# Optimization experiments

Hardware: AMD Instinct MI355X
Metric: run time of the kernel (lower is better)

## Reference

```python
import jax, jax.numpy as jnp
import numpy as np

B, H, S, DK = 2, 16, 2048, 64
NEG = jnp.float32(-10000.0)


def setup_inputs() -> dict:
    key = jax.random.key(0)
    kq, kk, kv, km = jax.random.split(key, 4)
    query = jax.random.normal(kq, (B, H, S, DK), dtype=jnp.float32)
    k_ = jax.random.normal(kk, (B, H, S, DK), dtype=jnp.float32)
    value = jax.random.normal(kv, (B, H, S, DK), dtype=jnp.float32)
    mask = (jax.random.uniform(km, (B, 1, S, S)) > 0.5).astype(jnp.float32)
    return {"query": query, "key": k_, "value": value, "mask": mask, "d_k": DK}


def reference(query, key, value, mask, d_k):
    # scores: [B,H,S,S]
    scale = jnp.float32(1.0 / np.sqrt(d_k))
    scores = jnp.einsum('bhqd,bhkd->bhqk', query, key) * scale * mask
    # non-standard masking: keep only strictly positive masked scores
    scores = jnp.where(scores > 0, scores, NEG)
    attn = jax.nn.softmax(scores, axis=-1)
    return jnp.einsum('bhqk,bhkd->bhqd', attn, value)
```

## Files before the change

### kernel.cpp

```cpp
#include <hip/hip_runtime.h>
#include <math.h>

#define S_LEN 2048
#define D_KV  64
#define BQ    128
#define BK    64
#define NT    (S_LEN / BK)

typedef __attribute__((ext_vector_type(8)))  short bh8;
typedef __attribute__((ext_vector_type(4)))  float fx4;
typedef __attribute__((ext_vector_type(16))) float fx16;
typedef __attribute__((ext_vector_type(4)))  unsigned int u32x4;
typedef __attribute__((ext_vector_type(2)))  unsigned int u32x2;

__device__ __forceinline__ unsigned cvt2(float a, float b) {
    unsigned r;
    asm("v_cvt_pk_bf16_f32 %0, %1, %2" : "=v"(r) : "v"(a), "v"(b));
    return r;
}
__device__ __forceinline__ void swap32(unsigned &d, unsigned &s) {
    asm("v_permlane32_swap_b32 %0, %1" : "+v"(d), "+v"(s));
}
__device__ __forceinline__ int swz(int row, int byteoff) {
    return (row << 7) + (byteoff ^ ((row & 7) << 4));
}

__global__ __launch_bounds__(256, 3)
void attn_fwd(const float* __restrict__ Qg, const float* __restrict__ Kg,
              const float* __restrict__ Vg, const float* __restrict__ Mg,
              float* __restrict__ Og)
{
    __shared__ __align__(16) char smem[16384];
    short* kb = (short*)smem;
    short* vb = (short*)(smem + 8192);

    const int tid  = threadIdx.x;
    const int lane = tid & 63;
    const int wave = tid >> 6;
    const int lq   = lane & 31;
    const int hf   = lane >> 5;

    const int flat = blockIdx.x + (int)gridDim.x * blockIdx.y;
    const int nsw  = (flat & 7) * 64 + (flat >> 3);
    const int qt = nsw & 15;
    const int bh = nsw >> 4;
    const int b  = bh >> 4;

    const int qbase = qt * BQ + wave * 32;

    const float* Kp = Kg + (size_t)bh * S_LEN * D_KV;
    const float* Vp = Vg + (size_t)bh * S_LEN * D_KV;
    const float* Qp = Qg + ((size_t)bh * S_LEN + qbase) * D_KV;
    const float* mrow = Mg + (size_t)b * S_LEN * S_LEN
                      + (size_t)(qbase + lq) * S_LEN + hf * 4;

    bh8 qf[4];
#pragma unroll
    for (int ks = 0; ks < 4; ++ks) {
        const float* src = Qp + lq * D_KV + ks * 16 + hf * 8;
        fx4 a0 = *(const fx4*)src;
        fx4 a1 = *(const fx4*)(src + 4);
        u32x4 q4 = { cvt2(a0[0] * 0.125f, a0[1] * 0.125f),
                     cvt2(a0[2] * 0.125f, a0[3] * 0.125f),
                     cvt2(a1[0] * 0.125f, a1[1] * 0.125f),
                     cvt2(a1[2] * 0.125f, a1[3] * 0.125f) };
        qf[ks] = __builtin_bit_cast(bh8, q4);
    }

    const int krow = tid >> 2;
    const int kcol = (tid & 3) << 2;
    const int vd0  = (tid >> 4) << 2;
    const int vk0  = (tid & 15) << 2;

    fx16 o0 = {}, o1 = {};
    float lsum = 0.f;
    fx4 kreg[4], vreg[4];

#pragma unroll
    for (int i = 0; i < 4; ++i)
        kreg[i] = *(const fx4*)(Kp + (size_t)krow * D_KV + kcol + 16 * i);
#pragma unroll
    for (int i = 0; i < 4; ++i)
        vreg[i] = *(const fx4*)(Vp + (size_t)(vk0 + i) * D_KV + vd0);

#pragma unroll 1
    for (int t = 0; t < NT; ++t) {
        const int kt = t * BK;

        fx4 mv0[4];
#pragma unroll
        for (int m = 0; m < 4; ++m)
            mv0[m] = *(const fx4*)(mrow + kt + m * 8);

#pragma unroll
        for (int i = 0; i < 4; ++i) {
            u32x2 w = { cvt2(kreg[i][0], kreg[i][1]),
                        cvt2(kreg[i][2], kreg[i][3]) };
            *(u32x2*)((char*)kb + swz(krow, (kcol << 1) + 32 * i)) = w;
        }
#pragma unroll
        for (int i = 0; i < 4; ++i) {
            u32x2 w = { cvt2(vreg[0][i], vreg[1][i]),
                        cvt2(vreg[2][i], vreg[3][i]) };
            *(u32x2*)((char*)vb + swz(vd0 + i, vk0 << 1)) = w;
        }
        __syncthreads();

        if (t + 1 < NT) {
            const int kn = kt + BK;
#pragma unroll
            for (int i = 0; i < 4; ++i)
                kreg[i] = *(const fx4*)(Kp + (size_t)(kn + krow) * D_KV + kcol + 16 * i);
#pragma unroll
            for (int i = 0; i < 4; ++i)
                vreg[i] = *(const fx4*)(Vp + (size_t)(kn + vk0 + i) * D_KV + vd0);
        }

        fx16 st0 = {}, st1 = {};
        __builtin_amdgcn_s_setprio(1);
#pragma unroll
        for (int ks = 0; ks < 4; ++ks) {
            bh8 k0 = *(const bh8*)((char*)kb + swz(lq,      ks * 32 + hf * 16));
            bh8 k1 = *(const bh8*)((char*)kb + swz(32 + lq, ks * 32 + hf * 16));
            st0 = __builtin_amdgcn_mfma_f32_32x32x16_bf16(k0, qf[ks], st0, 0, 0, 0);
            st1 = __builtin_amdgcn_mfma_f32_32x32x16_bf16(k1, qf[ks], st1, 0, 0, 0);
        }
        __builtin_amdgcn_s_setprio(0);

        fx4 mv1[4];
#pragma unroll
        for (int m = 0; m < 4; ++m)
            mv1[m] = *(const fx4*)(mrow + kt + 32 + m * 8);

        unsigned pkw[16];

#pragma unroll
        for (int m = 0; m < 4; ++m) {
            float tm0 = st0[4*m+0] * mv0[m][0];
            float tm1 = st0[4*m+1] * mv0[m][1];
            float tm2 = st0[4*m+2] * mv0[m][2];
            float tm3 = st0[4*m+3] * mv0[m][3];
            float p0 = tm0 > 0.f ? __expf(tm0) : 0.f;
            float p1 = tm1 > 0.f ? __expf(tm1) : 0.f;
            float p2 = tm2 > 0.f ? __expf(tm2) : 0.f;
            float p3 = tm3 > 0.f ? __expf(tm3) : 0.f;
            lsum += (p0 + p1) + (p2 + p3);
            pkw[m*2+0] = cvt2(p0, p1);
            pkw[m*2+1] = cvt2(p2, p3);
        }

        __builtin_amdgcn_s_setprio(1);
#pragma unroll
        for (int vp = 0; vp < 2; ++vp) {
            unsigned w0 = pkw[vp*4+0], w1 = pkw[vp*4+1];
            unsigned w2 = pkw[vp*4+2], w3 = pkw[vp*4+3];
            swap32(w0, w2); swap32(w1, w3);
            u32x4 pq = { w0, w1, w2, w3 };
            bh8 pb = __builtin_bit_cast(bh8, pq);
            bh8 v0 = *(const bh8*)((char*)vb + swz(lq,      vp * 32 + hf * 16));
            bh8 v1 = *(const bh8*)((char*)vb + swz(32 + lq, vp * 32 + hf * 16));
            o0 = __builtin_amdgcn_mfma_f32_32x32x16_bf16(v0, pb, o0, 0, 0, 0);
            o1 = __builtin_amdgcn_mfma_f32_32x32x16_bf16(v1, pb, o1, 0, 0, 0);
        }
        __builtin_amdgcn_s_setprio(0);

#pragma unroll
        for (int m = 0; m < 4; ++m) {
            float tm0 = st1[4*m+0] * mv1[m][0];
            float tm1 = st1[4*m+1] * mv1[m][1];
            float tm2 = st1[4*m+2] * mv1[m][2];
            float tm3 = st1[4*m+3] * mv1[m][3];
            float p0 = tm0 > 0.f ? __expf(tm0) : 0.f;
            float p1 = tm1 > 0.f ? __expf(tm1) : 0.f;
            float p2 = tm2 > 0.f ? __expf(tm2) : 0.f;
            float p3 = tm3 > 0.f ? __expf(tm3) : 0.f;
            lsum += (p0 + p1) + (p2 + p3);
            pkw[8 + m*2+0] = cvt2(p0, p1);
            pkw[8 + m*2+1] = cvt2(p2, p3);
        }

        __builtin_amdgcn_s_setprio(1);
#pragma unroll
        for (int vp = 2; vp < 4; ++vp) {
            unsigned w0 = pkw[vp*4+0], w1 = pkw[vp*4+1];
            unsigned w2 = pkw[vp*4+2], w3 = pkw[vp*4+3];
            swap32(w0, w2); swap32(w1, w3);
            u32x4 pq = { w0, w1, w2, w3 };
            bh8 pb = __builtin_bit_cast(bh8, pq);
            bh8 v0 = *(const bh8*)((char*)vb + swz(lq,      vp * 32 + hf * 16));
            bh8 v1 = *(const bh8*)((char*)vb + swz(32 + lq, vp * 32 + hf * 16));
            o0 = __builtin_amdgcn_mfma_f32_32x32x16_bf16(v0, pb, o0, 0, 0, 0);
            o1 = __builtin_amdgcn_mfma_f32_32x32x16_bf16(v1, pb, o1, 0, 0, 0);
        }
        __builtin_amdgcn_s_setprio(0);

        __syncthreads();
    }

    lsum += __shfl_xor(lsum, 32);
    const float inv = 1.0f / lsum;

    float* orow = Og + ((size_t)bh * S_LEN + qbase + lq) * D_KV;
#pragma unroll
    for (int m = 0; m < 4; ++m) {
        fx4 r0 = { o0[4*m+0]*inv, o0[4*m+1]*inv, o0[4*m+2]*inv, o0[4*m+3]*inv };
        *(fx4*)(orow + m * 8 + hf * 4) = r0;
        fx4 r1 = { o1[4*m+0]*inv, o1[4*m+1]*inv, o1[4*m+2]*inv, o1[4*m+3]*inv };
        *(fx4*)(orow + 32 + m * 8 + hf * 4) = r1;
    }
}

extern "C" void kernel_launch(void* const* d_in, const int* in_sizes, int n_in,
                              void* d_out, int out_size, void* d_ws, size_t ws_size,
                              hipStream_t stream) {
    const float* Q = (const float*)d_in[0];
    const float* K = (const float*)d_in[1];
    const float* V = (const float*)d_in[2];
    const float* M = (const float*)d_in[3];
    float*       O = (float*)d_out;
    dim3 grid(S_LEN / BQ, 32);
    attn_fwd<<<grid, 256, 0, stream>>>(Q, K, V, M, O);
}
```

Measured before the change: 234.8 us.

## Split KV range across two wave groups with double-buffered LDS and merge

After: 424.6 us. +80.8%, slower.

```diff
diff --git a/kernel.cpp b/kernel.cpp
--- a/kernel.cpp
+++ b/kernel.cpp
@@ -5,7 +5,8 @@
 #define D_KV  64
 #define BQ    128
 #define BK    64
-#define NT    (S_LEN / BK)
+#define KHALF 1024
+#define NT    (KHALF / BK)
 
 typedef __attribute__((ext_vector_type(8)))  short bh8;
 typedef __attribute__((ext_vector_type(4)))  float fx4;
@@ -21,22 +22,27 @@
 __device__ __forceinline__ void swap32(unsigned &d, unsigned &s) {
     asm("v_permlane32_swap_b32 %0, %1" : "+v"(d), "+v"(s));
 }
+__device__ __forceinline__ float exp2_fast(float x) {
+    float r;
+    asm("v_exp_f32 %0, %1" : "=v"(r) : "v"(x));
+    return r;
+}
 __device__ __forceinline__ int swz(int row, int byteoff) {
     return (row << 7) + (byteoff ^ ((row & 7) << 4));
 }
 
-__global__ __launch_bounds__(256, 3)
+__global__ __launch_bounds__(512, 4)
 void attn_fwd(const float* __restrict__ Qg, const float* __restrict__ Kg,
               const float* __restrict__ Vg, const float* __restrict__ Mg,
               float* __restrict__ Og)
 {
-    __shared__ __align__(16) char smem[16384];
-    short* kb = (short*)smem;
-    short* vb = (short*)(smem + 8192);
+    __shared__ __align__(16) char smem[65536];
 
     const int tid  = threadIdx.x;
     const int lane = tid & 63;
     const int wave = tid >> 6;
+    const int qw   = wave & 3;
+    const int kg   = wave >> 2;
     const int lq   = lane & 31;
     const int hf   = lane >> 5;
 
@@ -46,82 +52,91 @@
     const int bh = nsw >> 4;
     const int b  = bh >> 4;
 
-    const int qbase = qt * BQ + wave * 32;
-
-    const float* Kp = Kg + (size_t)bh * S_LEN * D_KV;
-    const float* Vp = Vg + (size_t)bh * S_LEN * D_KV;
+    const int qbase = qt * BQ + qw * 32;
+
+    const float* Kp = Kg + ((size_t)bh * S_LEN + kg * KHALF) * D_KV;
+    const float* Vp = Vg + ((size_t)bh * S_LEN + kg * KHALF) * D_KV;
     const float* Qp = Qg + ((size_t)bh * S_LEN + qbase) * D_KV;
     const float* mrow = Mg + (size_t)b * S_LEN * S_LEN
-                      + (size_t)(qbase + lq) * S_LEN + hf * 4;
-
+                      + (size_t)(qbase + lq) * S_LEN + kg * KHALF + hf * 4;
+
+    const float QS = 0.125f * 1.44269504f;
     bh8 qf[4];
 #pragma unroll
     for (int ks = 0; ks < 4; ++ks) {
         const float* src = Qp + lq * D_KV + ks * 16 + hf * 8;
         fx4 a0 = *(const fx4*)src;
         fx4 a1 = *(const fx4*)(src + 4);
-        u32x4 q4 = { cvt2(a0[0] * 0.125f, a0[1] * 0.125f),
-                     cvt2(a0[2] * 0.125f, a0[3] * 0.125f),
-                     cvt2(a1[0] * 0.125f, a1[1] * 0.125f),
-                     cvt2(a1[2] * 0.125f, a1[3] * 0.125f) };
+        u32x4 q4 = { cvt2(a0[0] * QS, a0[1] * QS),
+                     cvt2(a0[2] * QS, a0[3] * QS),
+                     cvt2(a1[0] * QS, a1[1] * QS),
+                     cvt2(a1[2] * QS, a1[3] * QS) };
         qf[ks] = __builtin_bit_cast(bh8, q4);
     }
 
-    const int krow = tid >> 2;
-    const int kcol = (tid & 3) << 2;
-    const int vd0  = (tid >> 4) << 2;
-    const int vk0  = (tid & 15) << 2;
+    const int stid  = tid & 255;
+    const int krow  = stid >> 2;
+    const int kcolf = (stid & 3) << 2;
+    const int vd0   = (stid >> 4) << 2;
+    const int vk0   = (stid & 15) << 2;
+
+    char* lbase = smem + kg * 32768;
+
+    fx4 kreg[4], vreg[4];
+    auto issue = [&](int t) {
+        const int k0 = t * BK;
+#pragma unroll
+        for (int i = 0; i < 4; ++i)
+            kreg[i] = *(const fx4*)(Kp + (size_t)(k0 + krow) * D_KV + kcolf + 16 * i);
+#pragma unroll
+        for (int i = 0; i < 4; ++i)
+            vreg[i] = *(const fx4*)(Vp + (size_t)(k0 + vk0 + i) * D_KV + vd0);
+    };
+    auto store_kv = [&](int buf) {
+        char* kbW = lbase + buf * 16384;
+        char* vbW = kbW + 8192;
+#pragma unroll
+        for (int i = 0; i < 4; ++i) {
+            u32x2 w = { cvt2(kreg[i][0], kreg[i][1]),
+                        cvt2(kreg[i][2], kreg[i][3]) };
+            *(u32x2*)(kbW + swz(krow, (kcolf << 1) + 32 * i)) = w;
+        }
+#pragma unroll
+        for (int i = 0; i < 4; ++i) {
+            u32x2 w = { cvt2(vreg[0][i], vreg[1][i]),
+                        cvt2(vreg[2][i], vreg[3][i]) };
+            *(u32x2*)(vbW + swz(vd0 + i, vk0 << 1)) = w;
+        }
+    };
 
     fx16 o0 = {}, o1 = {};
     float lsum = 0.f;
-    fx4 kreg[4], vreg[4];
-
-#pragma unroll
-    for (int i = 0; i < 4; ++i)
-        kreg[i] = *(const fx4*)(Kp + (size_t)krow * D_KV + kcol + 16 * i);
-#pragma unroll
-    for (int i = 0; i < 4; ++i)
-        vreg[i] = *(const fx4*)(Vp + (size_t)(vk0 + i) * D_KV + vd0);
+
+    issue(0);
+    store_kv(0);
+    issue(1);
+    asm volatile("s_waitcnt lgkmcnt(0)" ::: "memory");
+    __builtin_amdgcn_s_barrier();
 
 #pragma unroll 1
     for (int t = 0; t < NT; ++t) {
-        const int kt = t * BK;
+        char* kbR = lbase + (t & 1) * 16384;
+        char* vbR = kbR + 8192;
+        const int mc = t * BK;
 
         fx4 mv0[4];
 #pragma unroll
         for (int m = 0; m < 4; ++m)
-            mv0[m] = *(const fx4*)(mrow + kt + m * 8);
-
-#pragma unroll
-        for (int i = 0; i < 4; ++i) {
-            u32x2 w = { cvt2(kreg[i][0], kreg[i][1]),
-                        cvt2(kreg[i][2], kreg[i][3]) };
-            *(u32x2*)((char*)kb + swz(krow, (kcol << 1) + 32 * i)) = w;
-        }
-#pragma unroll
-        for (int i = 0; i < 4; ++i) {
-            u32x2 w = { cvt2(vreg[0][i], vreg[1][i]),
-                        cvt2(vreg[2][i], vreg[3][i]) };
-            *(u32x2*)((char*)vb + swz(vd0 + i, vk0 << 1)) = w;
-        }
-        __syncthreads();
-
-        if (t + 1 < NT) {
-            const int kn = kt + BK;
-#pragma unroll
-            for (int i = 0; i < 4; ++i)
-                kreg[i] = *(const fx4*)(Kp + (size_t)(kn + krow) * D_KV + kcol + 16 * i);
-#pragma unroll
-            for (int i = 0; i < 4; ++i)
-                vreg[i] = *(const fx4*)(Vp + (size_t)(kn + vk0 + i) * D_KV + vd0);
-        }
+            mv0[m] = *(const fx4*)(mrow + mc + m * 8);
+
+        if (t + 1 < NT) store_kv((t + 1) & 1);
 
         fx16 st0 = {}, st1 = {};
         __builtin_amdgcn_s_setprio(1);
 #pragma unroll
         for (int ks = 0; ks < 4; ++ks) {
-            bh8 k0 = *(const bh8*)((char*)kb + swz(lq,      ks * 32 + hf * 16));
-            bh8 k1 = *(const bh8*)((char*)kb + swz(32 + lq, ks * 32 + hf * 16));
+            bh8 k0 = *(const bh8*)(kbR + swz(lq,      ks * 32 + hf * 16));
+            bh8 k1 = *(const bh8*)(kbR + swz(32 + lq, ks * 32 + hf * 16));
             st0 = __builtin_amdgcn_mfma_f32_32x32x16_bf16(k0, qf[ks], st0, 0, 0, 0);
             st1 = __builtin_amdgcn_mfma_f32_32x32x16_bf16(k1, qf[ks], st1, 0, 0, 0);
         }
@@ -130,7 +145,8 @@
         fx4 mv1[4];
 #pragma unroll
         for (int m = 0; m < 4; ++m)
-            mv1[m] = *(const fx4*)(mrow + kt + 32 + m * 8);
+            mv1[m] = *(const fx4*)(mrow + mc + 32 + m * 8);
+        if (t + 2 < NT) issue(t + 2);
 
         unsigned pkw[16];
 
@@ -140,10 +156,10 @@
             float tm1 = st0[4*m+1] * mv0[m][1];
             float tm2 = st0[4*m+2] * mv0[m][2];
             float tm3 = st0[4*m+3] * mv0[m][3];
-            float p0 = tm0 > 0.f ? __expf(tm0) : 0.f;
-            float p1 = tm1 > 0.f ? __expf(tm1) : 0.f;
-            float p2 = tm2 > 0.f ? __expf(tm2) : 0.f;
-            float p3 = tm3 > 0.f ? __expf(tm3) : 0.f;
+            float p0 = tm0 > 0.f ? exp2_fast(tm0) : 0.f;
+            float p1 = tm1 > 0.f ? exp2_fast(tm1) : 0.f;
+            float p2 = tm2 > 0.f ? exp2_fast(tm2) : 0.f;
+            float p3 = tm3 > 0.f ? exp2_fast(tm3) : 0.f;
             lsum += (p0 + p1) + (p2 + p3);
             pkw[m*2+0] = cvt2(p0, p1);
             pkw[m*2+1] = cvt2(p2, p3);
@@ -157,8 +173,8 @@
             swap32(w0, w2); swap32(w1, w3);
             u32x4 pq = { w0, w1, w2, w3 };
             bh8 pb = __builtin_bit_cast(bh8, pq);
-            bh8 v0 = *(const bh8*)((char*)vb + swz(lq,      vp * 32 + hf * 16));
-            bh8 v1 = *(const bh8*)((char*)vb + swz(32 + lq, vp * 32 + hf * 16));
+            bh8 v0 = *(const bh8*)(vbR + swz(lq,      vp * 32 + hf * 16));
+            bh8 v1 = *(const bh8*)(vbR + swz(32 + lq, vp * 32 + hf * 16));
             o0 = __builtin_amdgcn_mfma_f32_32x32x16_bf16(v0, pb, o0, 0, 0, 0);
             o1 = __builtin_amdgcn_mfma_f32_32x32x16_bf16(v1, pb, o1, 0, 0, 0);
         }
@@ -170,10 +186,10 @@
             float tm1 = st1[4*m+1] * mv1[m][1];
             float tm2 = st1[4*m+2] * mv1[m][2];
             float tm3 = st1[4*m+3] * mv1[m][3];
-            float p0 = tm0 > 0.f ? __expf(tm0) : 0.f;
-            float p1 = tm1 > 0.f ? __expf(tm1) : 0.f;
-            float p2 = tm2 > 0.f ? __expf(tm2) : 0.f;
-            float p3 = tm3 > 0.f ? __expf(tm3) : 0.f;
+            float p0 = tm0 > 0.f ? exp2_fast(tm0) : 0.f;
+            float p1 = tm1 > 0.f ? exp2_fast(tm1) : 0.f;
+            float p2 = tm2 > 0.f ? exp2_fast(tm2) : 0.f;
+            float p3 = tm3 > 0.f ? exp2_fast(tm3) : 0.f;
             lsum += (p0 + p1) + (p2 + p3);
             pkw[8 + m*2+0] = cvt2(p0, p1);
             pkw[8 + m*2+1] = cvt2(p2, p3);
@@ -187,26 +203,55 @@
             swap32(w0, w2); swap32(w1, w3);
             u32x4 pq = { w0, w1, w2, w3 };
             bh8 pb = __builtin_bit_cast(bh8, pq);
-            bh8 v0 = *(const bh8*)((char*)vb + swz(lq,      vp * 32 + hf * 16));
-            bh8 v1 = *(const bh8*)((char*)vb + swz(32 + lq, vp * 32 + hf * 16));
+            bh8 v0 = *(const bh8*)(vbR + swz(lq,      vp * 32 + hf * 16));
+            bh8 v1 = *(const bh8*)(vbR + swz(32 + lq, vp * 32 + hf * 16));
             o0 = __builtin_amdgcn_mfma_f32_32x32x16_bf16(v0, pb, o0, 0, 0, 0);
             o1 = __builtin_amdgcn_mfma_f32_32x32x16_bf16(v1, pb, o1, 0, 0, 0);
         }
         __builtin_amdgcn_s_setprio(0);
 
-        __syncthreads();
+        asm volatile("s_waitcnt lgkmcnt(0)" ::: "memory");
+        __builtin_amdgcn_s_barrier();
     }
 
     lsum += __shfl_xor(lsum, 32);
-    const float inv = 1.0f / lsum;
-
-    float* orow = Og + ((size_t)bh * S_LEN + qbase + lq) * D_KV;
-#pragma unroll
-    for (int m = 0; m < 4; ++m) {
-        fx4 r0 = { o0[4*m+0]*inv, o0[4*m+1]*inv, o0[4*m+2]*inv, o0[4*m+3]*inv };
-        *(fx4*)(orow + m * 8 + hf * 4) = r0;
-        fx4 r1 = { o1[4*m+0]*inv, o1[4*m+1]*inv, o1[4*m+2]*inv, o1[4*m+3]*inv };
-        *(fx4*)(orow + 32 + m * 8 + hf * 4) = r1;
+
+    float* scr = (float*)smem;
+    const int slot = qw * 64 + lane;
+    if (kg) {
+        float* d = scr + slot * 36;
+#pragma unroll
+        for (int i = 0; i < 4; ++i) {
+            fx4 c0 = { o0[4*i+0], o0[4*i+1], o0[4*i+2], o0[4*i+3] };
+            *(fx4*)(d + 4 * i) = c0;
+            fx4 c1 = { o1[4*i+0], o1[4*i+1], o1[4*i+2], o1[4*i+3] };
+            *(fx4*)(d + 16 + 4 * i) = c1;
+        }
+        d[32] = lsum;
+    }
+    __syncthreads();
+    if (!kg) {
+        const float* s = scr + slot * 36;
+#pragma unroll
+        for (int i = 0; i < 4; ++i) {
+            fx4 c0 = *(const fx4*)(s + 4 * i);
+            o0[4*i+0] += c0[0]; o0[4*i+1] += c0[1];
+            o0[4*i+2] += c0[2]; o0[4*i+3] += c0[3];
+            fx4 c1 = *(const fx4*)(s + 16 + 4 * i);
+            o1[4*i+0] += c1[0]; o1[4*i+1] += c1[1];
+            o1[4*i+2] += c1[2]; o1[4*i+3] += c1[3];
+        }
+        lsum += s[32];
+        const float inv = 1.0f / lsum;
+
+        float* orow = Og + ((size_t)bh * S_LEN + qbase + lq) * D_KV;
+#pragma unroll
+        for (int m = 0; m < 4; ++m) {
+            fx4 r0 = { o0[4*m+0]*inv, o0[4*m+1]*inv, o0[4*m+2]*inv, o0[4*m+3]*inv };
+            *(fx4*)(orow + m * 8 + hf * 4) = r0;
+            fx4 r1 = { o1[4*m+0]*inv, o1[4*m+1]*inv, o1[4*m+2]*inv, o1[4*m+3]*inv };
+            *(fx4*)(orow + 32 + m * 8 + hf * 4) = r1;
+        }
     }
 }
 
@@ -219,5 +264,5 @@
     const float* M = (const float*)d_in[3];
     float*       O = (float*)d_out;
     dim3 grid(S_LEN / BQ, 32);
-    attn_fwd<<<grid, 256, 0, stream>>>(Q, K, V, M, O);
-}
+    attn_fwd<<<grid, 512, 0, stream>>>(Q, K, V, M, O);
+}
```

## Pack float mask into bitmask via pre-kernel and use exp2 with raw barriers

Applied to the files above, without the earlier changes.

After: 194.7 us. -17.1%, faster.

```diff
diff --git a/kernel.cpp b/kernel.cpp
--- a/kernel.cpp
+++ b/kernel.cpp
@@ -21,13 +21,34 @@
 __device__ __forceinline__ void swap32(unsigned &d, unsigned &s) {
     asm("v_permlane32_swap_b32 %0, %1" : "+v"(d), "+v"(s));
 }
+__device__ __forceinline__ float exp2_fast(float x) {
+    float r;
+    asm("v_exp_f32 %0, %1" : "=v"(r) : "v"(x));
+    return r;
+}
 __device__ __forceinline__ int swz(int row, int byteoff) {
     return (row << 7) + (byteoff ^ ((row & 7) << 4));
 }
 
+__global__ __launch_bounds__(256)
+void pack_mask(const float* __restrict__ M, unsigned long long* __restrict__ BM)
+{
+    const size_t i = (size_t)blockIdx.x * 256 + threadIdx.x;
+    const float v = M[i];
+    const unsigned long long bits = __ballot(v > 0.5f);
+    if ((threadIdx.x & 63) == 0) {
+        const size_t g = i >> 6;
+        const int col64 = (int)(g & 31);
+        const int row   = (int)((g >> 5) & 2047);
+        const int b     = (int)(g >> 16);
+        BM[((size_t)b * 32 + col64) * 2048 + row] = bits;
+    }
+}
+
 __global__ __launch_bounds__(256, 3)
 void attn_fwd(const float* __restrict__ Qg, const float* __restrict__ Kg,
-              const float* __restrict__ Vg, const float* __restrict__ Mg,
+              const float* __restrict__ Vg,
+              const unsigned long long* __restrict__ BMg,
               float* __restrict__ Og)
 {
     __shared__ __align__(16) char smem[16384];
@@ -51,19 +72,19 @@
     const float* Kp = Kg + (size_t)bh * S_LEN * D_KV;
     const float* Vp = Vg + (size_t)bh * S_LEN * D_KV;
     const float* Qp = Qg + ((size_t)bh * S_LEN + qbase) * D_KV;
-    const float* mrow = Mg + (size_t)b * S_LEN * S_LEN
-                      + (size_t)(qbase + lq) * S_LEN + hf * 4;
-
+    const unsigned long long* BMp = BMg + (size_t)b * 32 * 2048 + qbase + lq;
+
+    const float QS = 0.125f * 1.44269504f;
     bh8 qf[4];
 #pragma unroll
     for (int ks = 0; ks < 4; ++ks) {
         const float* src = Qp + lq * D_KV + ks * 16 + hf * 8;
         fx4 a0 = *(const fx4*)src;
         fx4 a1 = *(const fx4*)(src + 4);
-        u32x4 q4 = { cvt2(a0[0] * 0.125f, a0[1] * 0.125f),
-                     cvt2(a0[2] * 0.125f, a0[3] * 0.125f),
-                     cvt2(a1[0] * 0.125f, a1[1] * 0.125f),
-                     cvt2(a1[2] * 0.125f, a1[3] * 0.125f) };
+        u32x4 q4 = { cvt2(a0[0] * QS, a0[1] * QS),
+                     cvt2(a0[2] * QS, a0[3] * QS),
+                     cvt2(a1[0] * QS, a1[1] * QS),
+                     cvt2(a1[2] * QS, a1[3] * QS) };
         qf[ks] = __builtin_bit_cast(bh8, q4);
     }
 
@@ -76,21 +97,20 @@
     float lsum = 0.f;
     fx4 kreg[4], vreg[4];
 
-#pragma unroll
-    for (int i = 0; i < 4; ++i)
-        kreg[i] = *(const fx4*)(Kp + (size_t)krow * D_KV + kcol + 16 * i);
-#pragma unroll
-    for (int i = 0; i < 4; ++i)
-        vreg[i] = *(const fx4*)(Vp + (size_t)(vk0 + i) * D_KV + vd0);
+    auto issue = [&](int kt) {
+#pragma unroll
+        for (int i = 0; i < 4; ++i)
+            kreg[i] = *(const fx4*)(Kp + (size_t)(kt + krow) * D_KV + kcol + 16 * i);
+#pragma unroll
+        for (int i = 0; i < 4; ++i)
+            vreg[i] = *(const fx4*)(Vp + (size_t)(kt + vk0 + i) * D_KV + vd0);
+    };
+
+    issue(0);
 
 #pragma unroll 1
     for (int t = 0; t < NT; ++t) {
-        const int kt = t * BK;
-
-        fx4 mv0[4];
-#pragma unroll
-        for (int m = 0; m < 4; ++m)
-            mv0[m] = *(const fx4*)(mrow + kt + m * 8);
+        const unsigned long long bm = BMp[(size_t)t * 2048];
 
 #pragma unroll
         for (int i = 0; i < 4; ++i) {
@@ -104,17 +124,10 @@
                         cvt2(vreg[2][i], vreg[3][i]) };
             *(u32x2*)((char*)vb + swz(vd0 + i, vk0 << 1)) = w;
         }
-        __syncthreads();
-
-        if (t + 1 < NT) {
-            const int kn = kt + BK;
-#pragma unroll
-            for (int i = 0; i < 4; ++i)
-                kreg[i] = *(const fx4*)(Kp + (size_t)(kn + krow) * D_KV + kcol + 16 * i);
-#pragma unroll
-            for (int i = 0; i < 4; ++i)
-                vreg[i] = *(const fx4*)(Vp + (size_t)(kn + vk0 + i) * D_KV + vd0);
-        }
+        asm volatile("s_waitcnt lgkmcnt(0)" ::: "memory");
+        __builtin_amdgcn_s_barrier();
+
+        if (t + 1 < NT) issue((t + 1) * BK);
 
         fx16 st0 = {}, st1 = {};
         __builtin_amdgcn_s_setprio(1);
@@ -127,23 +140,20 @@
         }
         __builtin_amdgcn_s_setprio(0);
 
-        fx4 mv1[4];
-#pragma unroll
-        for (int m = 0; m < 4; ++m)
-            mv1[m] = *(const fx4*)(mrow + kt + 32 + m * 8);
+        const unsigned s0 = ((unsigned)bm) >> (hf * 4);
+        const unsigned s1 = ((unsigned)(bm >> 32)) >> (hf * 4);
 
         unsigned pkw[16];
 
 #pragma unroll
         for (int m = 0; m < 4; ++m) {
-            float tm0 = st0[4*m+0] * mv0[m][0];
-            float tm1 = st0[4*m+1] * mv0[m][1];
-            float tm2 = st0[4*m+2] * mv0[m][2];
-            float tm3 = st0[4*m+3] * mv0[m][3];
-            float p0 = tm0 > 0.f ? __expf(tm0) : 0.f;
-            float p1 = tm1 > 0.f ? __expf(tm1) : 0.f;
-            float p2 = tm2 > 0.f ? __expf(tm2) : 0.f;
-            float p3 = tm3 > 0.f ? __expf(tm3) : 0.f;
+            const unsigned bb = s0 >> (8 * m);
+            float tm0 = st0[4*m+0], tm1 = st0[4*m+1];
+            float tm2 = st0[4*m+2], tm3 = st0[4*m+3];
+            float p0 = ((bb      & 1) && tm0 > 0.f) ? exp2_fast(tm0) : 0.f;
+            float p1 = ((bb >> 1 & 1) && tm1 > 0.f) ? exp2_fast(tm1) : 0.f;
+            float p2 = ((bb >> 2 & 1) && tm2 > 0.f) ? exp2_fast(tm2) : 0.f;
+            float p3 = ((bb >> 3 & 1) && tm3 > 0.f) ? exp2_fast(tm3) : 0.f;
             lsum += (p0 + p1) + (p2 + p3);
             pkw[m*2+0] = cvt2(p0, p1);
             pkw[m*2+1] = cvt2(p2, p3);
@@ -166,14 +176,13 @@
 
 #pragma unroll
         for (int m = 0; m < 4; ++m) {
-            float tm0 = st1[4*m+0] * mv1[m][0];
-            float tm1 = st1[4*m+1] * mv1[m][1];
-            float tm2 = st1[4*m+2] * mv1[m][2];
-            float tm3 = st1[4*m+3] * mv1[m][3];
-            float p0 = tm0 > 0.f ? __expf(tm0) : 0.f;
-            float p1 = tm1 > 0.f ? __expf(tm1) : 0.f;
-            float p2 = tm2 > 0.f ? __expf(tm2) : 0.f;
-            float p3 = tm3 > 0.f ? __expf(tm3) : 0.f;
+            const unsigned bb = s1 >> (8 * m);
+            float tm0 = st1[4*m+0], tm1 = st1[4*m+1];
+            float tm2 = st1[4*m+2], tm3 = st1[4*m+3];
+            float p0 = ((bb      & 1) && tm0 > 0.f) ? exp2_fast(tm0) : 0.f;
+            float p1 = ((bb >> 1 & 1) && tm1 > 0.f) ? exp2_fast(tm1) : 0.f;
+            float p2 = ((bb >> 2 & 1) && tm2 > 0.f) ? exp2_fast(tm2) : 0.f;
+            float p3 = ((bb >> 3 & 1) && tm3 > 0.f) ? exp2_fast(tm3) : 0.f;
             lsum += (p0 + p1) + (p2 + p3);
             pkw[8 + m*2+0] = cvt2(p0, p1);
             pkw[8 + m*2+1] = cvt2(p2, p3);
@@ -194,7 +203,7 @@
         }
         __builtin_amdgcn_s_setprio(0);
 
-        __syncthreads();
+        __builtin_amdgcn_s_barrier();
     }
 
     lsum += __shfl_xor(lsum, 32);
@@ -218,6 +227,10 @@
     const float* V = (const float*)d_in[2];
     const float* M = (const float*)d_in[3];
     float*       O = (float*)d_out;
+    unsigned long long* BM = (unsigned long long*)d_ws;
+
+    pack_mask<<<dim3(32768), 256, 0, stream>>>(M, BM);
+
     dim3 grid(S_LEN / BQ, 32);
-    attn_fwd<<<grid, 256, 0, stream>>>(Q, K, V, M, O);
-}
+    attn_fwd<<<grid, 256, 0, stream>>>(Q, K, V, BM, O);
+}
```
